# Kernel optimization log

Measured on AMD Instinct MI355X. Metric: run time of the kernel, lower is better.

Reference implementation:

```python
import jax, jax.numpy as jnp
import numpy as np

V, H, B, T_ENC, S, T_DEC, G = 18000, 400, 16, 256, 30, 8, 3


def setup_inputs() -> dict:
    key = jax.random.key(0)
    ks = jax.random.split(key, 16)
    def n(k, shape, s=0.1):
        return jax.random.normal(k, shape, jnp.float32) * s
    return {
        'story': jax.random.randint(ks[0], (B, T_ENC), 0, V, dtype=jnp.int32),
        'target_batches': jax.random.randint(ks[1], (B, S, T_DEC), 0, V, dtype=jnp.int32),
        'emb': n(ks[2], (V, H)),
        'enc_Wih_f': n(ks[3], (3 * H, H)), 'enc_Whh_f': n(ks[4], (3 * H, H)),
        'enc_bih_f': jnp.zeros((3 * H,), jnp.float32), 'enc_bhh_f': jnp.zeros((3 * H,), jnp.float32),
        'enc_Wih_b': n(ks[5], (3 * H, H)), 'enc_Whh_b': n(ks[6], (3 * H, H)),
        'enc_bih_b': jnp.zeros((3 * H,), jnp.float32), 'enc_bhh_b': jnp.zeros((3 * H,), jnp.float32),
        'dec_Wih': n(ks[7], (3 * H, H)), 'dec_Whh': n(ks[8], (3 * H, H)),
        'dec_bih': jnp.zeros((3 * H,), jnp.float32), 'dec_bhh': jnp.zeros((3 * H,), jnp.float32),
        'W_ratio': n(ks[9], (1, 3 * H)), 'b_ratio': jnp.zeros((1,), jnp.float32),
        'W_gate': n(ks[10], (G, H)), 'b_gate': jnp.zeros((G,), jnp.float32),
        'slot_emb': n(ks[11], (S, H)),
    }


def _gru_step(h, x, Wih, Whh, bih, bhh):
    # PyTorch GRU gate order: r, z, n
    gi = x @ Wih.T + bih
    gh = h @ Whh.T + bhh
    ir, iz, ig = jnp.split(gi, 3, axis=-1)
    hr, hz, hg = jnp.split(gh, 3, axis=-1)
    r = jax.nn.sigmoid(ir + hr)
    z = jax.nn.sigmoid(iz + hz)
    g = jnp.tanh(ig + r * hg)
    return (1.0 - z) * g + z * h


def _run_gru(xs, h0, Wih, Whh, bih, bhh):
    def step(h, x):
        h2 = _gru_step(h, x, Wih, Whh, bih, bhh)
        return h2, h2
    hT, out = jax.lax.scan(step, h0, xs)
    return out, hT


def reference(story, target_batches, emb,
              enc_Wih_f, enc_Whh_f, enc_bih_f, enc_bhh_f,
              enc_Wih_b, enc_Whh_b, enc_bih_b, enc_bhh_b,
              dec_Wih, dec_Whh, dec_bih, dec_bhh,
              W_ratio, b_ratio, W_gate, b_gate, slot_emb):
    # ---- EncoderRNN (bidirectional 1-layer GRU; dropout=0 / eval mode) ----
    x = emb[story.T]                       # (T_enc, B, H)
    h0 = jnp.zeros((B, H), x.dtype)
    out_f, h_f = _run_gru(x, h0, enc_Wih_f, enc_Whh_f, enc_bih_f, enc_bhh_f)
    out_b_rev, h_b = _run_gru(x[::-1], h0, enc_Wih_b, enc_Whh_b, enc_bih_b, enc_bhh_b)
    out_b = out_b_rev[::-1]
    enc_out = jnp.transpose(out_f + out_b, (1, 0, 2))   # (B, T_enc, H) = fwd+bwd halves summed
    enc_hidden = h_f + h_b                               # (B, H)     = hidden[0] + hidden[1]

    # ---- Generator decode loop ----
    SB = S * B
    dec_in0 = jnp.broadcast_to(slot_emb[:, None, :], (S, B, H)).reshape(SB, H)
    h = jnp.tile(enc_hidden, (S, 1))                     # (SB, H)
    enc_tiled = jnp.tile(enc_out, (S, 1, 1))             # (SB, T_enc, H)
    story_tiled = jnp.tile(story, (S, 1))                # (SB, T_enc)
    rows = jnp.arange(SB)[:, None]
    # teacher-forcing tokens per step, slot-major flatten to (T_dec, SB)
    tf_tokens = jnp.transpose(target_batches, (2, 1, 0)).reshape(T_DEC, SB)

    def step(carry, tok):
        h, dec_in = carry
        h2 = _gru_step(h, dec_in, dec_Wih, dec_Whh, dec_bih, dec_bhh)  # dec_state == new hidden
        scores = jnp.einsum('nd,ntd->nt', h2, enc_tiled)               # attend (all lens == T_enc)
        prob = jax.nn.softmax(scores, axis=1)
        context = jnp.einsum('nt,ntd->nd', prob, enc_tiled)
        gate = context @ W_gate.T + b_gate                              # (SB, G)
        p_vocab = jax.nn.softmax(h2 @ emb.T, axis=1)                    # (SB, V)
        p_gen = jnp.concatenate([h2, context, dec_in], axis=-1)         # (SB, 3H)
        sw = jax.nn.sigmoid(p_gen @ W_ratio.T + b_ratio)                # (SB, 1)
        ptr = jnp.zeros((SB, V), prob.dtype).at[rows, story_tiled].add(prob)  # scatter_add copy dist
        final = (1.0 - sw) * ptr + sw * p_vocab
        dec_in_next = emb[tok]                                          # teacher forcing
        return (h2, dec_in_next), (final, gate)

    _, (finals, gates) = jax.lax.scan(step, (h, dec_in0), tf_tokens)
    all_pointer_outputs = finals.reshape(T_DEC, S, B, V).transpose(1, 2, 0, 3)  # (S, B, T_dec, V)
    all_gate_outputs = gates[0].reshape(S, B, G)                                 # gate from step 0
    return all_pointer_outputs, all_gate_outputs
```

## Files before the change

kernel.cpp:

```cpp
#include <hip/hip_runtime.h>
#include <cstdint>
#include <cstddef>

#define VV 18000
#define HH 400
#define H3 1200
#define H3P 1280
#define KP 416
#define BB 16
#define TE 256
#define SS 30
#define TDN 8
#define GGN 3
#define SBN 480
#define NROW_ENC 4096
#define VP 18048
#define MP_DEC 512

#define EBLK 25
#define GIDEC_TILES 300
#define EMBB_BLKS 256

typedef __bf16 bf16;
typedef __attribute__((ext_vector_type(8))) __bf16 bf16x8;
typedef __attribute__((ext_vector_type(4))) float f32x4;
typedef __attribute__((ext_vector_type(4))) unsigned int u32x4;

static __device__ __forceinline__ float sigf(float x) {
    return 1.0f / (1.0f + __expf(-x));
}

static __device__ void gemm_dev(const bf16* __restrict__ A, const bf16* __restrict__ B,
                                float* __restrict__ Cf, bf16* __restrict__ Ch,
                                int M, int N, int K, int m0, int n0) {
    __shared__ __align__(16) bf16 sA[128 * 32];
    __shared__ __align__(16) bf16 sB[128 * 32];
    const int tid = threadIdx.x;
    const int lane = tid & 63;
    const int wave = tid >> 6;
    const int wm = wave >> 1, wn = wave & 1;
    f32x4 acc[4][4] = {};
    const int c0 = tid, c1 = tid + 256;
    const int r0 = c0 >> 2, q0 = (c0 & 3) * 8;
    const int r1 = c1 >> 2, q1 = (c1 & 3) * 8;
    const int ar = lane & 15, ak = (lane >> 4) * 8;
    const int nk = K >> 5;
    for (int kt = 0; kt < nk; ++kt) {
        const int kb = kt * 32;
        uint4 a0 = *(const uint4*)(A + (size_t)(m0 + r0) * K + kb + q0);
        uint4 a1 = *(const uint4*)(A + (size_t)(m0 + r1) * K + kb + q1);
        uint4 b0 = *(const uint4*)(B + (size_t)(n0 + r0) * K + kb + q0);
        uint4 b1 = *(const uint4*)(B + (size_t)(n0 + r1) * K + kb + q1);
        __syncthreads();
        *(uint4*)(sA + r0 * 32 + q0) = a0;
        *(uint4*)(sA + r1 * 32 + q1) = a1;
        *(uint4*)(sB + r0 * 32 + q0) = b0;
        *(uint4*)(sB + r1 * 32 + q1) = b1;
        __syncthreads();
        bf16x8 af[4], bg[4];
#pragma unroll
        for (int i = 0; i < 4; ++i)
            af[i] = *(const bf16x8*)(sA + (wm * 64 + i * 16 + ar) * 32 + ak);
#pragma unroll
        for (int j = 0; j < 4; ++j)
            bg[j] = *(const bf16x8*)(sB + (wn * 64 + j * 16 + ar) * 32 + ak);
#pragma unroll
        for (int i = 0; i < 4; ++i)
#pragma unroll
            for (int j = 0; j < 4; ++j)
                acc[i][j] = __builtin_amdgcn_mfma_f32_16x16x32_bf16(af[i], bg[j], acc[i][j], 0, 0, 0);
    }
    const int cr = (lane >> 4) * 4, cc = lane & 15;
    if (Ch) {
#pragma unroll
        for (int i = 0; i < 4; ++i)
#pragma unroll
            for (int j = 0; j < 4; ++j)
#pragma unroll
                for (int q = 0; q < 4; ++q) {
                    int row = m0 + wm * 64 + i * 16 + cr + q;
                    int col = n0 + wn * 64 + j * 16 + cc;
                    Ch[(size_t)row * N + col] = (bf16)acc[i][j][q];
                }
    } else {
#pragma unroll
        for (int i = 0; i < 4; ++i)
#pragma unroll
            for (int j = 0; j < 4; ++j)
#pragma unroll
                for (int q = 0; q < 4; ++q) {
                    int row = m0 + wm * 64 + i * 16 + cr + q;
                    int col = n0 + wn * 64 + j * 16 + cc;
                    Cf[(size_t)row * N + col] = acc[i][j][q];
                }
    }
}

__global__ __launch_bounds__(256) void gemm_bt(const bf16* __restrict__ A,
                                               const bf16* __restrict__ B,
                                               float* __restrict__ Cf, bf16* __restrict__ Ch,
                                               int M, int N, int K) {
    gemm_dev(A, B, Cf, Ch, M, N, K, blockIdx.x * 128, blockIdx.y * 128);
}

__global__ void prep_pad_bf16(const float* __restrict__ src, bf16* __restrict__ dst,
                              int rows_real, int cols_real, int rows_pad, int cols_pad) {
    int idx = blockIdx.x * blockDim.x + threadIdx.x;
    int total = rows_pad * cols_pad;
    if (idx >= total) return;
    int r = idx / cols_pad, c = idx % cols_pad;
    float v = (r < rows_real && c < cols_real) ? src[(size_t)r * cols_real + c] : 0.f;
    dst[idx] = (bf16)v;
}

__global__ void prep_aenc(const int* __restrict__ story, const float* __restrict__ emb,
                          bf16* __restrict__ dst) {
    int idx = blockIdx.x * blockDim.x + threadIdx.x;
    if (idx >= NROW_ENC * KP) return;
    int m = idx / KP, k = idx % KP;
    int t = m >> 4, b = m & 15;
    float v = 0.f;
    if (k < HH) {
        int tok = story[b * TE + t];
        v = emb[(size_t)tok * HH + k];
    }
    dst[idx] = (bf16)v;
}

__global__ void prep_decx(const int* __restrict__ target, const float* __restrict__ emb,
                          const float* __restrict__ slot, float* __restrict__ xf,
                          bf16* __restrict__ xb) {
    int idx = blockIdx.x * blockDim.x + threadIdx.x;
    if (idx >= TDN * SBN * KP) return;
    int k = idx % KP;
    int nn = idx / KP;
    int n = nn % SBN;
    int td = nn / SBN;
    int s = n >> 4, b = n & 15;
    float v = 0.f;
    if (k < HH) {
        if (td == 0) v = slot[s * HH + k];
        else {
            int tok = target[(b * SS + s) * TDN + (td - 1)];
            v = emb[(size_t)tok * HH + k];
        }
        xf[((size_t)td * SBN + n) * HH + k] = v;
    }
    xb[idx] = (bf16)v;
}

__global__ void zero_bf16k(bf16* dst, size_t total) {
    size_t idx = (size_t)blockIdx.x * blockDim.x + threadIdx.x;
    if (idx < total) dst[idx] = (bf16)0.f;
}

__global__ __launch_bounds__(256) void enc_fat(
    const float* __restrict__ gi_f, const float* __restrict__ gi_b,
    const float* __restrict__ whh_f, const float* __restrict__ whh_b,
    const float* __restrict__ bih_f, const float* __restrict__ bhh_f,
    const float* __restrict__ bih_b, const float* __restrict__ bhh_b,
    float* __restrict__ hist_f, float* __restrict__ hist_b,
    unsigned int* __restrict__ hbuf_f, unsigned int* __restrict__ hbuf_b,
    unsigned int* __restrict__ flags,
    const bf16* __restrict__ decxb, const bf16* __restrict__ dwihb,
    float* __restrict__ gidec,
    const float* __restrict__ emb, bf16* __restrict__ embb) {
    const int bid = blockIdx.x;
    const int tid = threadIdx.x;

    if (bid >= 2 * EBLK) {
        if (bid < 2 * EBLK + GIDEC_TILES) {
            int t = bid - 2 * EBLK;
            gemm_dev(decxb, dwihb, gidec, nullptr, TDN * SBN, H3P, KP,
                     (t % 30) * 128, (t / 30) * 128);
        } else {
            const size_t total = (size_t)VP * KP;
            size_t idx = (size_t)(bid - 2 * EBLK - GIDEC_TILES) * 256 + tid;
            const size_t stride = (size_t)EMBB_BLKS * 256;
            for (; idx < total; idx += stride) {
                int r = (int)(idx / KP), c = (int)(idx % KP);
                float v = (r < VV && c < HH) ? emb[(size_t)r * HH + c] : 0.f;
                embb[idx] = (bf16)v;
            }
        }
        return;
    }

    const int dir = bid & 1;
    const int blk = bid >> 1;
    const int j0 = blk * 16;
    const float* gi  = dir ? gi_b : gi_f;
    const float* whh = dir ? whh_b : whh_f;
    const float* bih = dir ? bih_b : bih_f;
    const float* bhh = dir ? bhh_b : bhh_f;
    float* hist = dir ? hist_b : hist_f;
    unsigned int* hbuf = dir ? hbuf_b : hbuf_f;

    __shared__ float GHL[3 * 256];

    const int wv = tid >> 6, lane = tid & 63;
    const int ub = tid >> 4, ucol = tid & 15;
    const int uj = j0 + ucol;
    const float bihr = bih[uj], bihz = bih[HH + uj], bihg = bih[2 * HH + uj];
    const float bhhr = bhh[uj], bhhz = bhh[HH + uj], bhhg = bhh[2 * HH + uj];

    const int kk0 = (lane >> 4) * 8;
    bf16x8 Bf[13];
    if (wv < 3) {
        const int brow = wv * HH + j0 + (lane & 15);
#pragma unroll
        for (int ks = 0; ks < 13; ++ks) {
            bf16x8 v;
#pragma unroll
            for (int e = 0; e < 8; ++e) {
                int k = kk0 + ks * 32 + e;
                v[e] = (k < HH) ? (bf16)whh[(size_t)brow * HH + k] : (bf16)0.f;
            }
            Bf[ks] = v;
        }
    }

    union UV { unsigned int d[4]; bf16x8 v; };

    float hp = 0.f;

    for (int s = 0; s < TE; ++s) {
        const int tt = dir ? (TE - 1 - s) : s;
        const float* gir = gi + ((size_t)tt * BB + ub) * H3P;
        float gi0 = gir[uj];
        float gi1 = gir[HH + uj];
        float gi2 = gir[2 * HH + uj];

        f32x4 acc0 = {}, acc1 = {};
        if (s > 0) {
            if (wv == 0) {
                const unsigned int* fl = flags + ((size_t)dir * TE + (s - 1)) * 32;
                while (true) {
                    unsigned f = 1u;
                    if (lane < EBLK)
                        asm volatile("global_load_dword %0, %1, off sc0 sc1"
                                     : "=v"(f) : "v"(fl + lane));
                    asm volatile("s_waitcnt vmcnt(0)" ::: "memory");
                    if (__all((int)(f != 0u))) break;
                }
            }
            __syncthreads();
            if (wv < 3) {
                const int ttp = dir ? (tt + 1) : (tt - 1);
                const unsigned int* hrow =
                    hbuf + ((size_t)ttp * BB + (lane & 15)) * KP + kk0;
                u32x4 ua[13], ubv[13];
#pragma unroll
                for (int ks = 0; ks < 13; ++ks) {
                    asm volatile("global_load_dwordx4 %0, %1, off offset:%c2 sc0 sc1"
                                 : "=v"(ua[ks]) : "v"(hrow), "n"(ks * 128));
                    asm volatile("global_load_dwordx4 %0, %1, off offset:%c2 sc0 sc1"
                                 : "=v"(ubv[ks]) : "v"(hrow), "n"(ks * 128 + 16));
                }
                asm volatile("s_waitcnt vmcnt(0)" ::: "memory");
                __builtin_amdgcn_sched_barrier(0);
#pragma unroll
                for (int ks = 0; ks < 13; ++ks) {
                    u32x4 a = ua[ks], b = ubv[ks];
                    UV ah, al;
                    ah.d[0] = (a.x & 0xffffu) | (a.y << 16);
                    ah.d[1] = (a.z & 0xffffu) | (a.w << 16);
                    ah.d[2] = (b.x & 0xffffu) | (b.y << 16);
                    ah.d[3] = (b.z & 0xffffu) | (b.w << 16);
                    al.d[0] = (a.x >> 16) | (a.y & 0xffff0000u);
                    al.d[1] = (a.z >> 16) | (a.w & 0xffff0000u);
                    al.d[2] = (b.x >> 16) | (b.y & 0xffff0000u);
                    al.d[3] = (b.z >> 16) | (b.w & 0xffff0000u);
                    acc0 = __builtin_amdgcn_mfma_f32_16x16x32_bf16(ah.v, Bf[ks], acc0, 0, 0, 0);
                    acc1 = __builtin_amdgcn_mfma_f32_16x16x32_bf16(al.v, Bf[ks], acc1, 0, 0, 0);
                }
            }
        }
        if (wv < 3) {
            f32x4 at = acc0 + acc1;
            const int cb0 = wv * 256 + ((lane >> 4) * 4) * 16 + (lane & 15);
            GHL[cb0]      = at[0];
            GHL[cb0 + 16] = at[1];
            GHL[cb0 + 32] = at[2];
            GHL[cb0 + 48] = at[3];
        }
        __syncthreads();

        float ghr = GHL[tid];
        float ghz = GHL[256 + tid];
        float ghg = GHL[512 + tid];
        float r = sigf(gi0 + bihr + ghr + bhhr);
        float z = sigf(gi1 + bihz + ghz + bhhz);
        float g = tanhf(gi2 + bihg + r * (ghg + bhhg));
        float hn = (1.f - z) * g + z * hp;
        hp = hn;
        hist[((size_t)tt * BB + ub) * HH + uj] = hn;
        bf16 hi = (bf16)hn;
        bf16 lo = (bf16)(hn - (float)hi);
        unsigned int pk = (unsigned int)__builtin_bit_cast(unsigned short, hi)
                        | ((unsigned int)__builtin_bit_cast(unsigned short, lo) << 16);
        unsigned int* hw = hbuf + ((size_t)tt * BB + ub) * KP + uj;
        asm volatile("global_store_dword %0, %1, off sc0 sc1" :: "v"(hw), "v"(pk) : "memory");

        asm volatile("s_waitcnt vmcnt(0)" ::: "memory");
        __syncthreads();
        if (tid == 0) {
            unsigned int one = 1u;
            unsigned int* fw = flags + ((size_t)dir * TE + s) * 32 + blk;
            asm volatile("global_store_dword %0, %1, off sc0 sc1" :: "v"(fw), "v"(one) : "memory");
        }
    }
}

__global__ void combine_enc(const float* __restrict__ hf, const float* __restrict__ hb,
                            float* __restrict__ enc_out) {
    int idx = blockIdx.x * blockDim.x + threadIdx.x;
    if (idx >= BB * TE * HH) return;
    int hcol = idx % HH;
    int t = (idx / HH) % TE;
    int b = idx / (HH * TE);
    size_t src = ((size_t)t * BB + b) * HH + hcol;
    enc_out[idx] = hf[src] + hb[src];
}

__global__ void init_hdec2(const float* __restrict__ hf, const float* __restrict__ hb,
                           float* __restrict__ hdec, bf16* __restrict__ h2b) {
    int idx = blockIdx.x * blockDim.x + threadIdx.x;
    if (idx >= SBN * HH) return;
    int hcol = idx % HH;
    int n = idx / HH;
    int b = n & 15;
    float v = hf[((size_t)(TE - 1) * BB + b) * HH + hcol] + hb[((size_t)b) * HH + hcol];
    hdec[idx] = v;
    h2b[(size_t)n * KP + hcol] = (bf16)v;
}

__global__ void gru_dec2(const float* __restrict__ gi, const float* __restrict__ gh,
                         const float* __restrict__ bih, const float* __restrict__ bhh,
                         const float* __restrict__ hprev, float* __restrict__ hnew,
                         bf16* __restrict__ h2b) {
    int idx = blockIdx.x * blockDim.x + threadIdx.x;
    if (idx >= SBN * HH) return;
    int n = idx / HH, j = idx % HH;
    const float* gir = gi + (size_t)n * H3P;
    const float* ghr = gh + (size_t)n * H3P;
    float r = sigf(gir[j] + bih[j] + ghr[j] + bhh[j]);
    float z = sigf(gir[HH + j] + bih[HH + j] + ghr[HH + j] + bhh[HH + j]);
    float g = tanhf(gir[2 * HH + j] + bih[2 * HH + j] + r * (ghr[2 * HH + j] + bhh[2 * HH + j]));
    float hn = (1.f - z) * g + z * hprev[idx];
    hnew[idx] = hn;
    h2b[(size_t)n * KP + j] = (bf16)hn;
}

__global__ __launch_bounds__(256) void attn3(
    const float* __restrict__ hfall,
    const float* __restrict__ enc,
    const float* __restrict__ decxf,
    const float* __restrict__ Wr, const float* __restrict__ br,
    const float* __restrict__ Wg, const float* __restrict__ bg,
    float* __restrict__ probw,
    float* __restrict__ sww,
    float* __restrict__ outg) {
    const int b = blockIdx.x >> 1;
    const int half = blockIdx.x & 1;
    const int td = blockIdx.y;
    const int s0 = half * 15;
    const int tid = threadIdx.x;
    const int lane = tid & 63, wv = tid >> 6;

    __shared__ __align__(16) float h2L[15][HH];
    __shared__ __align__(16) float scL[15][TE];
    __shared__ __align__(16) float cxL[15][HH];

    const float* h2base = hfall + (size_t)(td + 1) * SBN * HH;
    for (int i = tid; i < 15 * HH; i += 256) {
        int j = i / HH, k = i % HH;
        int n = (s0 + j) * BB + b;
        h2L[j][k] = h2base[(size_t)n * HH + k];
    }
    __syncthreads();

    {
        float acc[15];
#pragma unroll
        for (int j = 0; j < 15; ++j) acc[j] = 0.f;
        const float4* er = (const float4*)(enc + ((size_t)b * TE + tid) * HH);
        for (int k4 = 0; k4 < HH / 4; ++k4) {
            float4 e = er[k4];
#pragma unroll
            for (int j = 0; j < 15; ++j) {
                float4 hv = *(const float4*)(&h2L[j][k4 * 4]);
                acc[j] += e.x * hv.x + e.y * hv.y + e.z * hv.z + e.w * hv.w;
            }
        }
#pragma unroll
        for (int j = 0; j < 15; ++j) scL[j][tid] = acc[j];
    }
    __syncthreads();

    for (int j = wv; j < 15; j += 4) {
        float v0 = scL[j][lane], v1 = scL[j][lane + 64];
        float v2 = scL[j][lane + 128], v3 = scL[j][lane + 192];
        float m = fmaxf(fmaxf(v0, v1), fmaxf(v2, v3));
        for (int d = 32; d; d >>= 1) m = fmaxf(m, __shfl_xor(m, d));
        v0 = __expf(v0 - m); v1 = __expf(v1 - m);
        v2 = __expf(v2 - m); v3 = __expf(v3 - m);
        float s = v0 + v1 + v2 + v3;
        for (int d = 32; d; d >>= 1) s += __shfl_xor(s, d);
        float inv = 1.f / s;
        scL[j][lane]       = v0 * inv;
        scL[j][lane + 64]  = v1 * inv;
        scL[j][lane + 128] = v2 * inv;
        scL[j][lane + 192] = v3 * inv;
    }
    __syncthreads();

    for (int i = tid; i < 15 * TE; i += 256) {
        int j = i / TE, t = i % TE;
        int n = (s0 + j) * BB + b;
        probw[((size_t)td * SBN + n) * TE + t] = scL[j][t];
    }

    {
        float cx0[15], cx1[15];
#pragma unroll
        for (int j = 0; j < 15; ++j) { cx0[j] = 0.f; cx1[j] = 0.f; }
        const int c0 = tid, c1 = tid + 256;
        const bool has2 = (c1 < HH);
        for (int t = 0; t < TE; t += 2) {
            const float* e0r = enc + ((size_t)b * TE + t) * HH;
            const float* e1r = e0r + HH;
            float e00 = e0r[c0], e01 = e1r[c0];
            float e10 = 0.f, e11 = 0.f;
            if (has2) { e10 = e0r[c1]; e11 = e1r[c1]; }
#pragma unroll
            for (int j = 0; j < 15; ++j) {
                float2 p = *(const float2*)(&scL[j][t]);
                cx0[j] += p.x * e00 + p.y * e01;
                cx1[j] += p.x * e10 + p.y * e11;
            }
        }
#pragma unroll
        for (int j = 0; j < 15; ++j) {
            cxL[j][c0] = cx0[j];
            if (has2) cxL[j][c1] = cx1[j];
        }
    }
    __syncthreads();

    for (int j = wv; j < 15; j += 4) {
        int n = (s0 + j) * BB + b;
        const float* dx = decxf + ((size_t)td * SBN + n) * HH;
        float a = 0.f;
        for (int k = lane; k < H3; k += 64) {
            float v = (k < HH) ? h2L[j][k]
                    : (k < 2 * HH) ? cxL[j][k - HH]
                    : dx[k - 2 * HH];
            a += v * Wr[k];
        }
        for (int d = 32; d; d >>= 1) a += __shfl_xor(a, d);
        if (lane == 0) sww[(size_t)td * SBN + n] = sigf(a + br[0]);
    }

    if (td == 0) {
        for (int j = wv; j < 15; j += 4) {
            int n = (s0 + j) * BB + b;
#pragma unroll
            for (int g = 0; g < GGN; ++g) {
                float a = 0.f;
                for (int k = lane; k < HH; k += 64) a += cxL[j][k] * Wg[g * HH + k];
                for (int d = 32; d; d >>= 1) a += __shfl_xor(a, d);
                if (lane == 0) outg[n * GGN + g] = a + bg[g];
            }
        }
    }
}

__global__ __launch_bounds__(1024) void smax_scatter3(
    const bf16* __restrict__ logitsH, const float* __restrict__ sw,
    const int* __restrict__ story, const float* __restrict__ probw,
    float* __restrict__ out, int td0) {
    int n = blockIdx.x, tid = threadIdx.x;
    int td = td0 + blockIdx.y;
    const bf16* lrow = logitsH + ((size_t)blockIdx.y * MP_DEC + n) * VP;
    const float* prow = probw + ((size_t)td * SBN + n) * TE;
    float swv = sw[(size_t)td * SBN + n];
    __shared__ float red[16];
    __shared__ float bc[2];
    float v[18];
    float mx = -1e30f;
#pragma unroll
    for (int i = 0; i < 18; ++i) {
        int c = tid + (i << 10);
        v[i] = (c < VV) ? (float)lrow[c] : -1e30f;
        mx = fmaxf(mx, v[i]);
    }
    for (int d = 32; d; d >>= 1) mx = fmaxf(mx, __shfl_xor(mx, d));
    if ((tid & 63) == 0) red[tid >> 6] = mx;
    __syncthreads();
    if (tid == 0) {
        float m2 = red[0];
        for (int w = 1; w < 16; ++w) m2 = fmaxf(m2, red[w]);
        bc[0] = m2;
    }
    __syncthreads();
    mx = bc[0];
    float s = 0.f;
#pragma unroll
    for (int i = 0; i < 18; ++i) {
        int c = tid + (i << 10);
        if (c < VV) { v[i] = __expf(v[i] - mx); s += v[i]; }
    }
    for (int d = 32; d; d >>= 1) s += __shfl_xor(s, d);
    if ((tid & 63) == 0) red[tid >> 6] = s;
    __syncthreads();
    if (tid == 0) {
        float s2 = 0.f;
        for (int w = 0; w < 16; ++w) s2 += red[w];
        bc[1] = s2;
    }
    __syncthreads();
    float scale = swv / bc[1];
    float* orow = out + ((size_t)n * TDN + td) * VV;
#pragma unroll
    for (int i = 0; i < 18; ++i) {
        int c = tid + (i << 10);
        if (c < VV) orow[c] = v[i] * scale;
    }
    __syncthreads();
    if (tid < TE) {
        int b = n & 15;
        int tok = story[b * TE + tid];
        float val = (1.f - swv) * prow[tid];
        atomicAdd(orow + tok, val);
    }
}

static inline int cdiv(long long a, long long b) { return (int)((a + b - 1) / b); }

extern "C" void kernel_launch(void* const* d_in, const int* in_sizes, int n_in,
                              void* d_out, int out_size, void* d_ws, size_t ws_size,
                              hipStream_t stream) {
    const int*   story  = (const int*)d_in[0];
    const int*   target = (const int*)d_in[1];
    const float* emb    = (const float*)d_in[2];
    const float* wih_f  = (const float*)d_in[3];
    const float* whh_f  = (const float*)d_in[4];
    const float* bih_f  = (const float*)d_in[5];
    const float* bhh_f  = (const float*)d_in[6];
    const float* wih_b  = (const float*)d_in[7];
    const float* whh_b  = (const float*)d_in[8];
    const float* bih_b  = (const float*)d_in[9];
    const float* bhh_b  = (const float*)d_in[10];
    const float* dwih   = (const float*)d_in[11];
    const float* dwhh   = (const float*)d_in[12];
    const float* dbih   = (const float*)d_in[13];
    const float* dbhh   = (const float*)d_in[14];
    const float* wr     = (const float*)d_in[15];
    const float* brr    = (const float*)d_in[16];
    const float* wgg    = (const float*)d_in[17];
    const float* bgg    = (const float*)d_in[18];
    const float* slot   = (const float*)d_in[19];
    float* out = (float*)d_out;

    char* wsb = (char*)d_ws;
    size_t off = 0;
    auto alloc = [&](size_t bytes) -> char* {
        char* p = wsb + off;
        off = (off + bytes + 255) & ~(size_t)255;
        return p;
    };
    bf16*  embb  = (bf16*)alloc((size_t)VP * KP * 2);
    bf16*  aenc  = (bf16*)alloc((size_t)NROW_ENC * KP * 2);
    bf16*  wfb   = (bf16*)alloc((size_t)H3P * KP * 2);
    bf16*  wbb   = (bf16*)alloc((size_t)H3P * KP * 2);
    bf16*  dwihb = (bf16*)alloc((size_t)H3P * KP * 2);
    bf16*  dwhhb = (bf16*)alloc((size_t)H3P * KP * 2);
    bf16*  decxb = (bf16*)alloc((size_t)TDN * SBN * KP * 2);
    bf16*  h2ball= (bf16*)alloc((size_t)9 * MP_DEC * KP * 2);
    unsigned int* hbuff = (unsigned int*)alloc((size_t)TE * BB * KP * 4);
    unsigned int* hbufb = (unsigned int*)alloc((size_t)TE * BB * KP * 4);
    unsigned int* flags = (unsigned int*)alloc((size_t)2 * TE * 32 * 4);
    float* gif   = (float*)alloc((size_t)NROW_ENC * H3P * 4);
    float* gib   = (float*)alloc((size_t)NROW_ENC * H3P * 4);
    float* gidec = (float*)alloc((size_t)TDN * SBN * H3P * 4);
    float* ghdec = (float*)alloc((size_t)MP_DEC * H3P * 4);
    float* histf = (float*)alloc((size_t)TE * BB * HH * 4);
    float* histb = (float*)alloc((size_t)TE * BB * HH * 4);
    float* encout= (float*)alloc((size_t)BB * TE * HH * 4);
    float* decxf = (float*)alloc((size_t)TDN * SBN * HH * 4);
    float* hfall = (float*)alloc((size_t)9 * SBN * HH * 4);
    float* probw = (float*)alloc((size_t)TDN * SBN * TE * 4);
    float* sww   = (float*)alloc((size_t)TDN * SBN * 4);
    bf16*  logitsH = (bf16*)alloc((size_t)MP_DEC * VP * 2);
    const size_t bigBytes = (size_t)TDN * MP_DEC * VP * 2;
    bf16* logitsAllH = nullptr;
    if (off + bigBytes + 256 <= ws_size) logitsAllH = (bf16*)alloc(bigBytes);
    (void)in_sizes; (void)n_in; (void)out_size;

    (void)hipMemsetAsync(flags, 0, (size_t)2 * TE * 32 * 4, stream);

    const int thr = 256;
    prep_aenc<<<cdiv((long long)NROW_ENC * KP, thr), thr, 0, stream>>>(story, emb, aenc);
    prep_pad_bf16<<<cdiv((long long)H3P * KP, thr), thr, 0, stream>>>(wih_f, wfb, H3, HH, H3P, KP);
    prep_pad_bf16<<<cdiv((long long)H3P * KP, thr), thr, 0, stream>>>(wih_b, wbb, H3, HH, H3P, KP);
    prep_pad_bf16<<<cdiv((long long)H3P * KP, thr), thr, 0, stream>>>(dwih, dwihb, H3, HH, H3P, KP);
    prep_pad_bf16<<<cdiv((long long)H3P * KP, thr), thr, 0, stream>>>(dwhh, dwhhb, H3, HH, H3P, KP);
    prep_decx<<<cdiv((long long)TDN * SBN * KP, thr), thr, 0, stream>>>(target, emb, slot, decxf, decxb);
    zero_bf16k<<<cdiv((long long)9 * MP_DEC * KP, thr), thr, 0, stream>>>(h2ball, (size_t)9 * MP_DEC * KP);

    {
        dim3 g(NROW_ENC / 128, H3P / 128);
        gemm_bt<<<g, 256, 0, stream>>>(aenc, wfb, gif, nullptr, NROW_ENC, H3P, KP);
        gemm_bt<<<g, 256, 0, stream>>>(aenc, wbb, gib, nullptr, NROW_ENC, H3P, KP);
    }

    enc_fat<<<2 * EBLK + GIDEC_TILES + EMBB_BLKS, 256, 0, stream>>>(
        gif, gib, whh_f, whh_b, bih_f, bhh_f, bih_b, bhh_b,
        histf, histb, hbuff, hbufb, flags,
        decxb, dwihb, gidec, emb, embb);

    combine_enc<<<cdiv((long long)BB * TE * HH, thr), thr, 0, stream>>>(histf, histb, encout);
    init_hdec2<<<cdiv((long long)SBN * HH, thr), thr, 0, stream>>>(histf, histb, hfall, h2ball);

    for (int td = 0; td < TDN; ++td) {
        dim3 g(MP_DEC / 128, H3P / 128);
        gemm_bt<<<g, 256, 0, stream>>>(h2ball + (size_t)td * MP_DEC * KP, dwhhb, ghdec, nullptr,
                                       MP_DEC, H3P, KP);
        gru_dec2<<<cdiv((long long)SBN * HH, thr), thr, 0, stream>>>(
            gidec + (size_t)td * SBN * H3P, ghdec, dbih, dbhh,
            hfall + (size_t)td * SBN * HH,
            hfall + (size_t)(td + 1) * SBN * HH,
            h2ball + (size_t)(td + 1) * MP_DEC * KP);
    }

    {
        dim3 g(32, TDN);
        attn3<<<g, 256, 0, stream>>>(hfall, encout, decxf, wr, brr, wgg, bgg,
                                     probw, sww, out + (size_t)SBN * TDN * VV);
    }

    if (logitsAllH) {
        dim3 g((TDN * MP_DEC) / 128, VP / 128);
        gemm_bt<<<g, 256, 0, stream>>>(h2ball + (size_t)MP_DEC * KP, embb, nullptr, logitsAllH,
                                       TDN * MP_DEC, VP, KP);
        dim3 gs(SBN, TDN);
        smax_scatter3<<<gs, 1024, 0, stream>>>(logitsAllH, sww, story, probw, out, 0);
    } else {
        for (int td = 0; td < TDN; ++td) {
            dim3 g(MP_DEC / 128, VP / 128);
            gemm_bt<<<g, 256, 0, stream>>>(h2ball + (size_t)(td + 1) * MP_DEC * KP, embb,
                                           nullptr, logitsH, MP_DEC, VP, KP);
            dim3 gs(SBN, 1);
            smax_scatter3<<<gs, 1024, 0, stream>>>(logitsH, sww, story, probw, out, td);
        }
    }
}
```

Baseline: 1.710 ms.

## Fuse encoder input GEMMs into recurrent kernel with per-tile readiness flags

Moves the two encoder input-projection GEMMs into the persistent enc_fat launch as extra blocks. Each block publishes a per-tile flag with system-coherent stores, and the recurrent blocks spin on those flags before consuming each 8-timestep row chunk. The backward direction's tiles are ordered from the end so both recurrences can start as early as possible. The seven prep kernels are merged into one grid-stride kernel, and combine_enc and init_hdec2 are merged into one, which cuts launch count. The cost is flag spinning, a dependence on the recurrent blocks being co-resident with the GEMM blocks (risk of deadlock), and extra register and control complexity in the GEMM epilogue.

```diff
diff --git a/kernel.cpp b/kernel.cpp
--- a/kernel.cpp
+++ b/kernel.cpp
@@ -18,6 +18,7 @@
 #define MP_DEC 512
 
 #define EBLK 25
+#define GI_TILES 320
 #define GIDEC_TILES 300
 #define EMBB_BLKS 256
 
@@ -32,7 +33,7 @@
 
 static __device__ void gemm_dev(const bf16* __restrict__ A, const bf16* __restrict__ B,
                                 float* __restrict__ Cf, bf16* __restrict__ Ch,
-                                int M, int N, int K, int m0, int n0) {
+                                int M, int N, int K, int m0, int n0, int cmode) {
     __shared__ __align__(16) bf16 sA[128 * 32];
     __shared__ __align__(16) bf16 sB[128 * 32];
     const int tid = threadIdx.x;
@@ -71,97 +72,86 @@
                 acc[i][j] = __builtin_amdgcn_mfma_f32_16x16x32_bf16(af[i], bg[j], acc[i][j], 0, 0, 0);
     }
     const int cr = (lane >> 4) * 4, cc = lane & 15;
-    if (Ch) {
-#pragma unroll
-        for (int i = 0; i < 4; ++i)
-#pragma unroll
-            for (int j = 0; j < 4; ++j)
-#pragma unroll
-                for (int q = 0; q < 4; ++q) {
-                    int row = m0 + wm * 64 + i * 16 + cr + q;
-                    int col = n0 + wn * 64 + j * 16 + cc;
-                    Ch[(size_t)row * N + col] = (bf16)acc[i][j][q];
+#pragma unroll
+    for (int i = 0; i < 4; ++i)
+#pragma unroll
+        for (int j = 0; j < 4; ++j)
+#pragma unroll
+            for (int q = 0; q < 4; ++q) {
+                int row = m0 + wm * 64 + i * 16 + cr + q;
+                int col = n0 + wn * 64 + j * 16 + cc;
+                float v = acc[i][j][q];
+                if (cmode == 1) {
+                    Ch[(size_t)row * N + col] = (bf16)v;
+                } else if (cmode == 2) {
+                    float* p = Cf + (size_t)row * N + col;
+                    asm volatile("global_store_dword %0, %1, off sc0 sc1"
+                                 :: "v"(p), "v"(v) : "memory");
+                } else {
+                    Cf[(size_t)row * N + col] = v;
                 }
-    } else {
-#pragma unroll
-        for (int i = 0; i < 4; ++i)
-#pragma unroll
-            for (int j = 0; j < 4; ++j)
-#pragma unroll
-                for (int q = 0; q < 4; ++q) {
-                    int row = m0 + wm * 64 + i * 16 + cr + q;
-                    int col = n0 + wn * 64 + j * 16 + cc;
-                    Cf[(size_t)row * N + col] = acc[i][j][q];
-                }
-    }
+            }
 }
 
 __global__ __launch_bounds__(256) void gemm_bt(const bf16* __restrict__ A,
                                                const bf16* __restrict__ B,
                                                float* __restrict__ Cf, bf16* __restrict__ Ch,
-                                               int M, int N, int K) {
-    gemm_dev(A, B, Cf, Ch, M, N, K, blockIdx.x * 128, blockIdx.y * 128);
-}
-
-__global__ void prep_pad_bf16(const float* __restrict__ src, bf16* __restrict__ dst,
-                              int rows_real, int cols_real, int rows_pad, int cols_pad) {
-    int idx = blockIdx.x * blockDim.x + threadIdx.x;
-    int total = rows_pad * cols_pad;
-    if (idx >= total) return;
-    int r = idx / cols_pad, c = idx % cols_pad;
-    float v = (r < rows_real && c < cols_real) ? src[(size_t)r * cols_real + c] : 0.f;
-    dst[idx] = (bf16)v;
-}
-
-__global__ void prep_aenc(const int* __restrict__ story, const float* __restrict__ emb,
-                          bf16* __restrict__ dst) {
-    int idx = blockIdx.x * blockDim.x + threadIdx.x;
-    if (idx >= NROW_ENC * KP) return;
-    int m = idx / KP, k = idx % KP;
-    int t = m >> 4, b = m & 15;
-    float v = 0.f;
-    if (k < HH) {
-        int tok = story[b * TE + t];
-        v = emb[(size_t)tok * HH + k];
-    }
-    dst[idx] = (bf16)v;
-}
-
-__global__ void prep_decx(const int* __restrict__ target, const float* __restrict__ emb,
-                          const float* __restrict__ slot, float* __restrict__ xf,
-                          bf16* __restrict__ xb) {
-    int idx = blockIdx.x * blockDim.x + threadIdx.x;
-    if (idx >= TDN * SBN * KP) return;
-    int k = idx % KP;
-    int nn = idx / KP;
-    int n = nn % SBN;
-    int td = nn / SBN;
-    int s = n >> 4, b = n & 15;
-    float v = 0.f;
-    if (k < HH) {
-        if (td == 0) v = slot[s * HH + k];
-        else {
-            int tok = target[(b * SS + s) * TDN + (td - 1)];
-            v = emb[(size_t)tok * HH + k];
-        }
-        xf[((size_t)td * SBN + n) * HH + k] = v;
-    }
-    xb[idx] = (bf16)v;
-}
-
-__global__ void zero_bf16k(bf16* dst, size_t total) {
-    size_t idx = (size_t)blockIdx.x * blockDim.x + threadIdx.x;
-    if (idx < total) dst[idx] = (bf16)0.f;
+                                               int M, int N, int K, int cmode) {
+    gemm_dev(A, B, Cf, Ch, M, N, K, blockIdx.x * 128, blockIdx.y * 128, cmode);
+}
+
+__global__ void prep_all(const int* __restrict__ story, const int* __restrict__ target,
+                         const float* __restrict__ emb, const float* __restrict__ slot,
+                         const float* __restrict__ wih_f, const float* __restrict__ wih_b,
+                         const float* __restrict__ dwih, const float* __restrict__ dwhh,
+                         bf16* __restrict__ aenc,
+                         bf16* __restrict__ wfb, bf16* __restrict__ wbb,
+                         bf16* __restrict__ dwihb, bf16* __restrict__ dwhhb,
+                         float* __restrict__ decxf, bf16* __restrict__ decxb,
+                         bf16* __restrict__ h2ball) {
+    const size_t gid = (size_t)blockIdx.x * blockDim.x + threadIdx.x;
+    const size_t gs = (size_t)gridDim.x * blockDim.x;
+    for (size_t i = gid; i < (size_t)NROW_ENC * KP; i += gs) {
+        int m = (int)(i / KP), k = (int)(i % KP);
+        int t = m >> 4, b = m & 15;
+        float v = 0.f;
+        if (k < HH) v = emb[(size_t)story[b * TE + t] * HH + k];
+        aenc[i] = (bf16)v;
+    }
+    for (size_t i = gid; i < (size_t)H3P * KP; i += gs) {
+        int r = (int)(i / KP), c = (int)(i % KP);
+        bool in = (r < H3 && c < HH);
+        wfb[i]   = (bf16)(in ? wih_f[(size_t)r * HH + c] : 0.f);
+        wbb[i]   = (bf16)(in ? wih_b[(size_t)r * HH + c] : 0.f);
+        dwihb[i] = (bf16)(in ? dwih[(size_t)r * HH + c] : 0.f);
+        dwhhb[i] = (bf16)(in ? dwhh[(size_t)r * HH + c] : 0.f);
+    }
+    for (size_t i = gid; i < (size_t)TDN * SBN * KP; i += gs) {
+        int k = (int)(i % KP);
+        int nn = (int)(i / KP);
+        int n = nn % SBN;
+        int td = nn / SBN;
+        int s = n >> 4, b = n & 15;
+        float v = 0.f;
+        if (k < HH) {
+            if (td == 0) v = slot[s * HH + k];
+            else v = emb[(size_t)target[(b * SS + s) * TDN + (td - 1)] * HH + k];
+            decxf[((size_t)td * SBN + n) * HH + k] = v;
+        }
+        decxb[i] = (bf16)v;
+    }
+    for (size_t i = gid; i < (size_t)9 * MP_DEC * KP; i += gs) h2ball[i] = (bf16)0.f;
 }
 
 __global__ __launch_bounds__(256) void enc_fat(
-    const float* __restrict__ gi_f, const float* __restrict__ gi_b,
+    float* __restrict__ gif, float* __restrict__ gib,
     const float* __restrict__ whh_f, const float* __restrict__ whh_b,
     const float* __restrict__ bih_f, const float* __restrict__ bhh_f,
     const float* __restrict__ bih_b, const float* __restrict__ bhh_b,
     float* __restrict__ hist_f, float* __restrict__ hist_b,
     unsigned int* __restrict__ hbuf_f, unsigned int* __restrict__ hbuf_b,
-    unsigned int* __restrict__ flags,
+    unsigned int* __restrict__ flags, unsigned int* __restrict__ gflags,
+    const bf16* __restrict__ aenc, const bf16* __restrict__ wfb, const bf16* __restrict__ wbb,
     const bf16* __restrict__ decxb, const bf16* __restrict__ dwihb,
     float* __restrict__ gidec,
     const float* __restrict__ emb, bf16* __restrict__ embb) {
@@ -169,13 +159,29 @@
     const int tid = threadIdx.x;
 
     if (bid >= 2 * EBLK) {
-        if (bid < 2 * EBLK + GIDEC_TILES) {
-            int t = bid - 2 * EBLK;
+        int hb = bid - 2 * EBLK;
+        if (hb < 2 * GI_TILES) {
+            const int dir = hb >= GI_TILES;
+            int t = hb - dir * GI_TILES;
+            const int mrow = dir ? (31 - t / 10) : (t / 10);
+            const int ncol = t % 10;
+            gemm_dev(aenc, dir ? wbb : wfb, dir ? gib : gif, nullptr,
+                     NROW_ENC, H3P, KP, mrow * 128, ncol * 128, 2);
+            asm volatile("s_waitcnt vmcnt(0)" ::: "memory");
+            __syncthreads();
+            if (tid == 0) {
+                unsigned one = 1u;
+                unsigned* fw = gflags + ((size_t)dir * 32 + mrow) * 16 + ncol;
+                asm volatile("global_store_dword %0, %1, off sc0 sc1"
+                             :: "v"(fw), "v"(one) : "memory");
+            }
+        } else if (hb < 2 * GI_TILES + GIDEC_TILES) {
+            int t = hb - 2 * GI_TILES;
             gemm_dev(decxb, dwihb, gidec, nullptr, TDN * SBN, H3P, KP,
-                     (t % 30) * 128, (t / 30) * 128);
+                     (t % 30) * 128, (t / 30) * 128, 0);
         } else {
             const size_t total = (size_t)VP * KP;
-            size_t idx = (size_t)(bid - 2 * EBLK - GIDEC_TILES) * 256 + tid;
+            size_t idx = (size_t)(hb - 2 * GI_TILES - GIDEC_TILES) * 256 + tid;
             const size_t stride = (size_t)EMBB_BLKS * 256;
             for (; idx < total; idx += stride) {
                 int r = (int)(idx / KP), c = (int)(idx % KP);
@@ -189,7 +195,7 @@
     const int dir = bid & 1;
     const int blk = bid >> 1;
     const int j0 = blk * 16;
-    const float* gi  = dir ? gi_b : gi_f;
+    const float* gi  = dir ? gib : gif;
     const float* whh = dir ? whh_b : whh_f;
     const float* bih = dir ? bih_b : bih_f;
     const float* bhh = dir ? bhh_b : bhh_f;
@@ -203,6 +209,7 @@
     const int uj = j0 + ucol;
     const float bihr = bih[uj], bihz = bih[HH + uj], bihg = bih[2 * HH + uj];
     const float bhhr = bhh[uj], bhhz = bhh[HH + uj], bhhg = bhh[2 * HH + uj];
+    const int c0t = (j0) >> 7, c1t = (400 + j0) >> 7, c2t = (800 + j0) >> 7;
 
     const int kk0 = (lane >> 4) * 8;
     bf16x8 Bf[13];
@@ -223,9 +230,28 @@
     union UV { unsigned int d[4]; bf16x8 v; };
 
     float hp = 0.f;
+    int gwm = -1;
 
     for (int s = 0; s < TE; ++s) {
         const int tt = dir ? (TE - 1 - s) : s;
+        const int mrow = tt >> 3;
+        if (mrow != gwm) {
+            gwm = mrow;
+            if (wv == 0) {
+                const unsigned* gf = gflags + ((size_t)dir * 32 + mrow) * 16;
+                while (true) {
+                    unsigned f = 1u;
+                    if (lane < 3) {
+                        const unsigned* ga = gf + (lane == 0 ? c0t : lane == 1 ? c1t : c2t);
+                        asm volatile("global_load_dword %0, %1, off sc0 sc1"
+                                     : "=v"(f) : "v"(ga));
+                    }
+                    asm volatile("s_waitcnt vmcnt(0)" ::: "memory");
+                    if (__all((int)(f != 0u))) break;
+                }
+            }
+            __syncthreads();
+        }
         const float* gir = gi + ((size_t)tt * BB + ub) * H3P;
         float gi0 = gir[uj];
         float gi1 = gir[HH + uj];
@@ -312,27 +338,26 @@
     }
 }
 
-__global__ void combine_enc(const float* __restrict__ hf, const float* __restrict__ hb,
-                            float* __restrict__ enc_out) {
-    int idx = blockIdx.x * blockDim.x + threadIdx.x;
-    if (idx >= BB * TE * HH) return;
-    int hcol = idx % HH;
-    int t = (idx / HH) % TE;
-    int b = idx / (HH * TE);
-    size_t src = ((size_t)t * BB + b) * HH + hcol;
-    enc_out[idx] = hf[src] + hb[src];
-}
-
-__global__ void init_hdec2(const float* __restrict__ hf, const float* __restrict__ hb,
-                           float* __restrict__ hdec, bf16* __restrict__ h2b) {
-    int idx = blockIdx.x * blockDim.x + threadIdx.x;
-    if (idx >= SBN * HH) return;
-    int hcol = idx % HH;
-    int n = idx / HH;
-    int b = n & 15;
-    float v = hf[((size_t)(TE - 1) * BB + b) * HH + hcol] + hb[((size_t)b) * HH + hcol];
-    hdec[idx] = v;
-    h2b[(size_t)n * KP + hcol] = (bf16)v;
+__global__ void combine_init(const float* __restrict__ hf, const float* __restrict__ hb,
+                             float* __restrict__ enc_out,
+                             float* __restrict__ hdec, bf16* __restrict__ h2b) {
+    const size_t gid = (size_t)blockIdx.x * blockDim.x + threadIdx.x;
+    const size_t gs = (size_t)gridDim.x * blockDim.x;
+    for (size_t i = gid; i < (size_t)BB * TE * HH; i += gs) {
+        int hcol = (int)(i % HH);
+        int t = (int)((i / HH) % TE);
+        int b = (int)(i / (HH * TE));
+        size_t src = ((size_t)t * BB + b) * HH + hcol;
+        enc_out[i] = hf[src] + hb[src];
+    }
+    for (size_t i = gid; i < (size_t)SBN * HH; i += gs) {
+        int hcol = (int)(i % HH);
+        int n = (int)(i / HH);
+        int b = n & 15;
+        float v = hf[((size_t)(TE - 1) * BB + b) * HH + hcol] + hb[((size_t)b) * HH + hcol];
+        hdec[i] = v;
+        h2b[(size_t)n * KP + hcol] = (bf16)v;
+    }
 }
 
 __global__ void gru_dec2(const float* __restrict__ gi, const float* __restrict__ gh,
@@ -580,7 +605,8 @@
     bf16*  h2ball= (bf16*)alloc((size_t)9 * MP_DEC * KP * 2);
     unsigned int* hbuff = (unsigned int*)alloc((size_t)TE * BB * KP * 4);
     unsigned int* hbufb = (unsigned int*)alloc((size_t)TE * BB * KP * 4);
-    unsigned int* flags = (unsigned int*)alloc((size_t)2 * TE * 32 * 4);
+    unsigned int* flags = (unsigned int*)alloc((size_t)(2 * TE * 32 + 2 * 32 * 16) * 4);
+    unsigned int* gflags = flags + 2 * TE * 32;
     float* gif   = (float*)alloc((size_t)NROW_ENC * H3P * 4);
     float* gib   = (float*)alloc((size_t)NROW_ENC * H3P * 4);
     float* gidec = (float*)alloc((size_t)TDN * SBN * H3P * 4);
@@ -598,35 +624,23 @@
     if (off + bigBytes + 256 <= ws_size) logitsAllH = (bf16*)alloc(bigBytes);
     (void)in_sizes; (void)n_in; (void)out_size;
 
-    (void)hipMemsetAsync(flags, 0, (size_t)2 * TE * 32 * 4, stream);
+    (void)hipMemsetAsync(flags, 0, (size_t)(2 * TE * 32 + 2 * 32 * 16) * 4, stream);
 
     const int thr = 256;
-    prep_aenc<<<cdiv((long long)NROW_ENC * KP, thr), thr, 0, stream>>>(story, emb, aenc);
-    prep_pad_bf16<<<cdiv((long long)H3P * KP, thr), thr, 0, stream>>>(wih_f, wfb, H3, HH, H3P, KP);
-    prep_pad_bf16<<<cdiv((long long)H3P * KP, thr), thr, 0, stream>>>(wih_b, wbb, H3, HH, H3P, KP);
-    prep_pad_bf16<<<cdiv((long long)H3P * KP, thr), thr, 0, stream>>>(dwih, dwihb, H3, HH, H3P, KP);
-    prep_pad_bf16<<<cdiv((long long)H3P * KP, thr), thr, 0, stream>>>(dwhh, dwhhb, H3, HH, H3P, KP);
-    prep_decx<<<cdiv((long long)TDN * SBN * KP, thr), thr, 0, stream>>>(target, emb, slot, decxf, decxb);
-    zero_bf16k<<<cdiv((long long)9 * MP_DEC * KP, thr), thr, 0, stream>>>(h2ball, (size_t)9 * MP_DEC * KP);
-
-    {
-        dim3 g(NROW_ENC / 128, H3P / 128);
-        gemm_bt<<<g, 256, 0, stream>>>(aenc, wfb, gif, nullptr, NROW_ENC, H3P, KP);
-        gemm_bt<<<g, 256, 0, stream>>>(aenc, wbb, gib, nullptr, NROW_ENC, H3P, KP);
-    }
-
-    enc_fat<<<2 * EBLK + GIDEC_TILES + EMBB_BLKS, 256, 0, stream>>>(
+    prep_all<<<1024, thr, 0, stream>>>(story, target, emb, slot, wih_f, wih_b, dwih, dwhh,
+                                       aenc, wfb, wbb, dwihb, dwhhb, decxf, decxb, h2ball);
+
+    enc_fat<<<2 * EBLK + 2 * GI_TILES + GIDEC_TILES + EMBB_BLKS, 256, 0, stream>>>(
         gif, gib, whh_f, whh_b, bih_f, bhh_f, bih_b, bhh_b,
-        histf, histb, hbuff, hbufb, flags,
-        decxb, dwihb, gidec, emb, embb);
-
-    combine_enc<<<cdiv((long long)BB * TE * HH, thr), thr, 0, stream>>>(histf, histb, encout);
-    init_hdec2<<<cdiv((long long)SBN * HH, thr), thr, 0, stream>>>(histf, histb, hfall, h2ball);
+        histf, histb, hbuff, hbufb, flags, gflags,
+        aenc, wfb, wbb, decxb, dwihb, gidec, emb, embb);
+
+    combine_init<<<512, thr, 0, stream>>>(histf, histb, encout, hfall, h2ball);
 
     for (int td = 0; td < TDN; ++td) {
         dim3 g(MP_DEC / 128, H3P / 128);
         gemm_bt<<<g, 256, 0, stream>>>(h2ball + (size_t)td * MP_DEC * KP, dwhhb, ghdec, nullptr,
-                                       MP_DEC, H3P, KP);
+                                       MP_DEC, H3P, KP, 0);
         gru_dec2<<<cdiv((long long)SBN * HH, thr), thr, 0, stream>>>(
             gidec + (size_t)td * SBN * H3P, ghdec, dbih, dbhh,
             hfall + (size_t)td * SBN * HH,
@@ -643,14 +657,14 @@
     if (logitsAllH) {
         dim3 g((TDN * MP_DEC) / 128, VP / 128);
         gemm_bt<<<g, 256, 0, stream>>>(h2ball + (size_t)MP_DEC * KP, embb, nullptr, logitsAllH,
-                                       TDN * MP_DEC, VP, KP);
+                                       TDN * MP_DEC, VP, KP, 1);
         dim3 gs(SBN, TDN);
         smax_scatter3<<<gs, 1024, 0, stream>>>(logitsAllH, sww, story, probw, out, 0);
     } else {
         for (int td = 0; td < TDN; ++td) {
             dim3 g(MP_DEC / 128, VP / 128);
             gemm_bt<<<g, 256, 0, stream>>>(h2ball + (size_t)(td + 1) * MP_DEC * KP, embb,
-                                           nullptr, logitsH, MP_DEC, VP, KP);
+                                           nullptr, logitsH, MP_DEC, VP, KP, 1);
             dim3 gs(SBN, 1);
             smax_scatter3<<<gs, 1024, 0, stream>>>(logitsH, sww, story, probw, out, td);
         }
```

Measured after the change: 1.914 ms. 11.9% more time.
